# Kernel optimization log

Measured on AMD Instinct MI355X. Metric: run time of the kernel, lower is better.

## Reference

```python
import jax, jax.numpy as jnp
import numpy as np
import math

B, S, D, H, DFF = 4, 2048, 1024, 16, 4096
DK = D // H
EPS = 1e-5


def setup_inputs() -> dict:
    key = jax.random.key(0)
    ks = jax.random.split(key, 12)
    sc = 0.02
    inp = {
        "x": jax.random.normal(ks[0], (B, S, D), dtype=jnp.float32),
        "mask": jnp.ones((B, 1, 1, S), dtype=jnp.int32),
        "Wq": jax.random.normal(ks[1], (D, D), jnp.float32) * sc,
        "bq": jnp.zeros((D,), jnp.float32),
        "Wk": jax.random.normal(ks[2], (D, D), jnp.float32) * sc,
        "bk": jnp.zeros((D,), jnp.float32),
        "Wv": jax.random.normal(ks[3], (D, D), jnp.float32) * sc,
        "bv": jnp.zeros((D,), jnp.float32),
        "Wo": jax.random.normal(ks[4], (D, D), jnp.float32) * sc,
        "bo": jnp.zeros((D,), jnp.float32),
        "ln1_g": jnp.ones((D,), jnp.float32),
        "ln1_b": jnp.zeros((D,), jnp.float32),
        "W1": jax.random.normal(ks[5], (D, DFF), jnp.float32) * sc,
        "b1": jnp.zeros((DFF,), jnp.float32),
        "W2": jax.random.normal(ks[6], (DFF, D), jnp.float32) * sc,
        "b2": jnp.zeros((D,), jnp.float32),
        "ln2_g": jnp.ones((D,), jnp.float32),
        "ln2_b": jnp.zeros((D,), jnp.float32),
    }
    return inp


def _layer_norm(x, g, b):
    m = jnp.mean(x, axis=-1, keepdims=True)
    v = jnp.mean(jnp.square(x - m), axis=-1, keepdims=True)
    return (x - m) * jax.lax.rsqrt(v + EPS) * g + b


def reference(x, mask, Wq, bq, Wk, bk, Wv, bv, Wo, bo,
              ln1_g, ln1_b, W1, b1, W2, b2, ln2_g, ln2_b):
    b_, s_, d_ = x.shape
    h_, dk_ = H, DK
    # --- pre-LN attention sublayer ---
    hidden = _layer_norm(x, ln1_g, ln1_b)
    q = (hidden @ Wq + bq).reshape(b_, s_, h_, dk_).transpose(0, 2, 1, 3)  # [B,H,S,dk]
    k = (hidden @ Wk + bk).reshape(b_, s_, h_, dk_).transpose(0, 2, 1, 3)  # [B,H,S,dk]
    # NOTE: original code passes value=key (the value projection is dead code),
    # so K is used both as keys and as values. Reproduced faithfully.
    scores = jnp.einsum("bhqd,bhkd->bhqk", q, k) / math.sqrt(dk_)  # [B,H,S,S]
    scores = jnp.where(mask == 0, jnp.float32(-1e9), scores)
    p_attn = jax.nn.softmax(scores, axis=-1)
    attn_out = jnp.einsum("bhqk,bhkd->bhqd", p_attn, k)  # values == k
    attn_out = attn_out.transpose(0, 2, 1, 3).reshape(b_, s_, d_)
    attn_out = attn_out @ Wo + bo
    x = x + attn_out  # residual (dropout is identity in eval)
    # --- pre-LN FFN sublayer ---
    hidden2 = _layer_norm(x, ln2_g, ln2_b)
    ff = jax.nn.gelu(hidden2 @ W1 + b1, approximate=False) @ W2 + b2
    return x + ff
```

## Files before the change

kernel.cpp:

```cpp
#include <hip/hip_runtime.h>
#include <hip/hip_bf16.h>
#include <math.h>

#define B_   4
#define S_   2048
#define D_   1024
#define H_   16
#define DK_  64
#define DFF_ 4096
#define M_   (B_*S_)

typedef __bf16 bf16;
typedef bf16 bf16x8 __attribute__((ext_vector_type(8)));
typedef bf16 bf16x4 __attribute__((ext_vector_type(4)));
typedef float f32x4 __attribute__((ext_vector_type(4)));

__device__ __forceinline__ void g2lds16(const void* g, void* l) {
  __builtin_amdgcn_global_load_lds(
      (__attribute__((address_space(1))) void*)(void*)g,
      (__attribute__((address_space(3))) void*)l, 16, 0, 0);
}

__device__ __forceinline__ void* swzp(char* base, int row, int byteofs) {
  return base + row * 128 + (byteofs ^ ((row & 7) << 4));
}

__global__ void tcast_all(const float* __restrict__ Wq, const float* __restrict__ Wk,
                          const float* __restrict__ Wo, const float* __restrict__ W1,
                          const float* __restrict__ W2,
                          bf16* __restrict__ WqkT, bf16* __restrict__ WoT,
                          bf16* __restrict__ W1T, bf16* __restrict__ W2T) {
  __shared__ float t[32][33];
  int bid = blockIdx.x;
  const float* src; bf16* dst; int K, N, bx, by;
  if (bid < 1024)      { src = Wq; dst = WqkT;            K = 1024; N = 1024; bx = bid & 31;  by = bid >> 5; }
  else if (bid < 2048) { bid -= 1024; src = Wk; dst = WqkT + 1024 * 1024; K = 1024; N = 1024; bx = bid & 31;  by = bid >> 5; }
  else if (bid < 3072) { bid -= 2048; src = Wo; dst = WoT; K = 1024; N = 1024; bx = bid & 31;  by = bid >> 5; }
  else if (bid < 7168) { bid -= 3072; src = W1; dst = W1T; K = 1024; N = 4096; bx = bid & 127; by = bid >> 7; }
  else                 { bid -= 7168; src = W2; dst = W2T; K = 4096; N = 1024; bx = bid & 31;  by = bid >> 5; }
  int n0 = bx * 32, k0 = by * 32;
  int tx = threadIdx.x, ty = threadIdx.y;
#pragma unroll
  for (int i = 0; i < 4; ++i)
    t[ty + i*8][tx] = src[(size_t)(k0 + ty + i*8) * N + n0 + tx];
  __syncthreads();
#pragma unroll
  for (int i = 0; i < 4; ++i)
    dst[(size_t)(n0 + ty + i*8) * K + k0 + tx] = (bf16)t[tx][ty + i*8];
}

__global__ __launch_bounds__(256)
void ktrans(const bf16* __restrict__ Kt, bf16* __restrict__ KT) {
  __shared__ bf16 t[64][72];
  const int bh = blockIdx.y, s0 = blockIdx.x * 64, tid = threadIdx.x;
  const bf16* src = Kt + (size_t)bh * S_ * DK_;
  bf16* dst = KT + (size_t)bh * DK_ * S_;
#pragma unroll
  for (int i = 0; i < 2; ++i) {
    int c = tid * 2 + i;
    int r = c >> 3, col = (c & 7) * 8;
    *(bf16x8*)&t[r][col] = *(const bf16x8*)&src[(size_t)(s0 + r) * 64 + col];
  }
  __syncthreads();
  const int d = tid >> 2, sc = (tid & 3) * 16;
  bf16x8 v0, v1;
#pragma unroll
  for (int j = 0; j < 8; ++j) { v0[j] = t[sc + j][d]; v1[j] = t[sc + 8 + j][d]; }
  *(bf16x8*)&dst[(size_t)d * S_ + s0 + sc] = v0;
  *(bf16x8*)&dst[(size_t)d * S_ + s0 + sc + 8] = v1;
}

__global__ __launch_bounds__(256)
void ln_fwd(const float* __restrict__ x, const float* __restrict__ g,
            const float* __restrict__ be, bf16* __restrict__ out) {
  int row = blockIdx.x, tid = threadIdx.x;
  const float4 v = *(const float4*)&x[(size_t)row * D_ + tid * 4];
  float s = v.x + v.y + v.z + v.w;
  float q = v.x*v.x + v.y*v.y + v.z*v.z + v.w*v.w;
#pragma unroll
  for (int d = 32; d; d >>= 1) { s += __shfl_down(s, d); q += __shfl_down(q, d); }
  __shared__ float red[8];
  int wave = tid >> 6, lane = tid & 63;
  if (lane == 0) { red[wave*2] = s; red[wave*2+1] = q; }
  __syncthreads();
  float ts = red[0] + red[2] + red[4] + red[6];
  float tq = red[1] + red[3] + red[5] + red[7];
  float mean = ts * (1.0f / D_);
  float var  = tq * (1.0f / D_) - mean * mean;
  float rstd = rsqrtf(var + 1e-5f);
  const float4 gg = *(const float4*)&g[tid * 4];
  const float4 bb = *(const float4*)&be[tid * 4];
  bf16x4 ov;
  ov[0] = (bf16)((v.x - mean) * rstd * gg.x + bb.x);
  ov[1] = (bf16)((v.y - mean) * rstd * gg.y + bb.y);
  ov[2] = (bf16)((v.z - mean) * rstd * gg.z + bb.z);
  ov[3] = (bf16)((v.w - mean) * rstd * gg.w + bb.w);
  *(bf16x4*)&out[(size_t)row * D_ + tid * 4] = ov;
}

template <int EPI>
__global__ __launch_bounds__(256)
void gemm_bt(const bf16* __restrict__ A, const bf16* __restrict__ Bt,
             int M, int N, int K,
             const float* __restrict__ bias, const float* __restrict__ bias2,
             const float* __restrict__ resid, float scale,
             float* __restrict__ outf, bf16* __restrict__ outb,
             bf16* __restrict__ outb2) {
  __shared__ __align__(16) bf16 As[128 * 32];
  __shared__ __align__(16) bf16 Bs[128 * 32];
  const int tid = threadIdx.x;
  const int wave = tid >> 6, lane = tid & 63;
  const int wr = wave >> 1, wc = wave & 1;

  const int gx = gridDim.x, nwg = gx * gridDim.y;
  int wg = blockIdx.y * gx + blockIdx.x;
  wg = (wg & 7) * (nwg >> 3) + (wg >> 3);
  const long arow = (long)(wg / gx) * 128;
  const long bcol = (long)(wg % gx) * 128;

  f32x4 acc[4][4] = {};

  const int c0 = wave * 2, c1 = wave * 2 + 1;
  const int srow0 = c0 * 16 + (lane >> 2);
  const int srow1 = c1 * 16 + (lane >> 2);
  const int scol = (lane & 3) * 8;
  const int l15 = lane & 15, kof = (lane >> 4) * 8;

  for (int k0 = 0; k0 < K; k0 += 32) {
    g2lds16(A  + (arow + srow0) * (long)K + k0 + scol, &As[c0 * 512]);
    g2lds16(A  + (arow + srow1) * (long)K + k0 + scol, &As[c1 * 512]);
    g2lds16(Bt + (bcol + srow0) * (long)K + k0 + scol, &Bs[c0 * 512]);
    g2lds16(Bt + (bcol + srow1) * (long)K + k0 + scol, &Bs[c1 * 512]);
    __syncthreads();
    bf16x8 a[4], b[4];
#pragma unroll
    for (int i = 0; i < 4; ++i)
      a[i] = *(const bf16x8*)&As[(wr * 64 + i * 16 + l15) * 32 + kof];
#pragma unroll
    for (int i = 0; i < 4; ++i)
      b[i] = *(const bf16x8*)&Bs[(wc * 64 + i * 16 + l15) * 32 + kof];
#pragma unroll
    for (int mi = 0; mi < 4; ++mi)
#pragma unroll
      for (int ni = 0; ni < 4; ++ni)
        acc[mi][ni] = __builtin_amdgcn_mfma_f32_16x16x32_bf16(
            a[mi], b[ni], acc[mi][ni], 0, 0, 0);
    __syncthreads();
  }

#pragma unroll
  for (int mi = 0; mi < 4; ++mi) {
#pragma unroll
    for (int ni = 0; ni < 4; ++ni) {
#pragma unroll
      for (int j = 0; j < 4; ++j) {
        long row = arow + wr * 64 + mi * 16 + (lane >> 4) * 4 + j;
        long col = bcol + wc * 64 + ni * 16 + l15;
        float v = acc[mi][ni][j];
        if constexpr (EPI == 0) {
          int bb = (int)(row >> 11), ss = (int)(row & 2047);
          int hh = (int)(col >> 6) & 15, dd = (int)(col & 63);
          size_t idx = (((size_t)(bb * H_ + hh)) * S_ + ss) * DK_ + dd;
          if (col < 1024) outb[idx]  = (bf16)((v + bias[col]) * scale);
          else            outb2[idx] = (bf16)(v + bias2[col - 1024]);
        } else if constexpr (EPI == 1) {
          size_t idx = (size_t)row * N + col;
          outf[idx] = v + bias[col] + resid[idx];
        } else {
          size_t idx = (size_t)row * N + col;
          float t = v + bias[col];
          outb[idx] = (bf16)(0.5f * t * (1.0f + erff(t * 0.70710678118654752f)));
        }
      }
    }
  }
}

__global__ __launch_bounds__(256)
void attn_fwd(const bf16* __restrict__ Q, const bf16* __restrict__ Kk,
              const bf16* __restrict__ KT, const int* __restrict__ mask,
              bf16* __restrict__ O) {
  __shared__ __align__(16) char Kl[64 * 128];
  __shared__ __align__(16) char Vl[64 * 128];
  __shared__ __align__(16) char Pl[4][16 * 128];

  const int tid = threadIdx.x, wave = tid >> 6, lane = tid & 63;
  const int bh = blockIdx.y, b = bh >> 4, h = bh & 15;
  const int q0 = blockIdx.x * 64;
  const int l15 = lane & 15, q4 = lane >> 4;

  const bf16* Qp = Q  + (size_t)bh * S_ * DK_;
  const bf16* Kp = Kk + (size_t)bh * S_ * DK_;
  const bf16* Tp = KT + (size_t)bh * DK_ * S_;

  const int qrow = q0 + wave * 16 + l15;
  const bf16x8 qf0 = *(const bf16x8*)&Qp[(size_t)qrow * 64 + q4 * 8];
  const bf16x8 qf1 = *(const bf16x8*)&Qp[(size_t)qrow * 64 + 32 + q4 * 8];

  const int c0 = tid * 2, c1 = tid * 2 + 1;
  const int sr0 = c0 >> 3, sb0 = c0 & 7;
  const int sr1 = c1 >> 3, sb1 = c1 & 7;

  int poff[16];
#pragma unroll
  for (int nt = 0; nt < 4; ++nt)
#pragma unroll
    for (int j = 0; j < 4; ++j) {
      int r = q4 * 4 + j;
      poff[nt * 4 + j] = r * 128 + ((((nt * 16 + l15) * 2)) ^ ((r & 7) << 4));
    }

  bf16x8 onesv;
#pragma unroll
  for (int i = 0; i < 8; ++i) onesv[i] = (bf16)1.0f;

  f32x4 o[4] = {};
  f32x4 ol = {};
  float m_r[4];
#pragma unroll
  for (int j = 0; j < 4; ++j) m_r[j] = -__builtin_inff();

  bf16x8 a0 = *(const bf16x8*)&Kp[(size_t)sr0 * 64 + sb0 * 8];
  bf16x8 a1 = *(const bf16x8*)&Kp[(size_t)sr1 * 64 + sb1 * 8];
  bf16x8 t0 = *(const bf16x8*)&Tp[(size_t)sr0 * S_ + sb0 * 8];
  bf16x8 t1 = *(const bf16x8*)&Tp[(size_t)sr1 * S_ + sb1 * 8];

  for (int k0 = 0; k0 < S_; k0 += 64) {
    *(bf16x8*)swzp(Kl, sr0, sb0 * 16) = a0;
    *(bf16x8*)swzp(Kl, sr1, sb1 * 16) = a1;
    *(bf16x8*)swzp(Vl, sr0, sb0 * 16) = t0;
    *(bf16x8*)swzp(Vl, sr1, sb1 * 16) = t1;
    __syncthreads();

    const int nk = k0 + 64;
    if (nk < S_) {
      a0 = *(const bf16x8*)&Kp[(size_t)(nk + sr0) * 64 + sb0 * 8];
      a1 = *(const bf16x8*)&Kp[(size_t)(nk + sr1) * 64 + sb1 * 8];
      t0 = *(const bf16x8*)&Tp[(size_t)sr0 * S_ + nk + sb0 * 8];
      t1 = *(const bf16x8*)&Tp[(size_t)sr1 * S_ + nk + sb1 * 8];
    }

    const int mv = mask[b * S_ + k0 + lane];
    const bool anyz = __any(mv == 0);

    f32x4 s[4];
#pragma unroll
    for (int nt = 0; nt < 4; ++nt) {
      bf16x8 kf0 = *(const bf16x8*)swzp(Kl, nt * 16 + l15, q4 * 16);
      bf16x8 kf1 = *(const bf16x8*)swzp(Kl, nt * 16 + l15, 64 + q4 * 16);
      f32x4 z = {};
      z     = __builtin_amdgcn_mfma_f32_16x16x32_bf16(qf0, kf0, z, 0, 0, 0);
      s[nt] = __builtin_amdgcn_mfma_f32_16x16x32_bf16(qf1, kf1, z, 0, 0, 0);
    }
    if (anyz) {
#pragma unroll
      for (int nt = 0; nt < 4; ++nt) {
        int m2 = mask[b * S_ + k0 + nt * 16 + l15];
        if (m2 == 0) {
#pragma unroll
          for (int j = 0; j < 4; ++j) s[nt][j] = -1e9f;
        }
      }
    }

    float tm[4];
#pragma unroll
    for (int j = 0; j < 4; ++j)
      tm[j] = fmaxf(fmaxf(s[0][j], s[1][j]), fmaxf(s[2][j], s[3][j]));
#pragma unroll
    for (int d = 1; d < 16; d <<= 1)
#pragma unroll
      for (int j = 0; j < 4; ++j)
        tm[j] = fmaxf(tm[j], __shfl_xor(tm[j], d));

    bool ok = true;
#pragma unroll
    for (int j = 0; j < 4; ++j) ok = ok && (tm[j] <= m_r[j] + 8.0f);
    if (!__all(ok)) {
#pragma unroll
      for (int j = 0; j < 4; ++j) {
        float mn = fmaxf(m_r[j], tm[j]);
        float sf = __builtin_amdgcn_exp2f(m_r[j] - mn);
        m_r[j] = mn;
        ol[j] *= sf;
#pragma unroll
        for (int nf = 0; nf < 4; ++nf) o[nf][j] *= sf;
      }
    }

#pragma unroll
    for (int nt = 0; nt < 4; ++nt)
#pragma unroll
      for (int j = 0; j < 4; ++j)
        *(bf16*)(&Pl[wave][0] + poff[nt * 4 + j]) =
            (bf16)__builtin_amdgcn_exp2f(s[nt][j] - m_r[j]);

    const bf16x8 pf0 = *(const bf16x8*)swzp(Pl[wave], l15, q4 * 16);
    const bf16x8 pf1 = *(const bf16x8*)swzp(Pl[wave], l15, 64 + q4 * 16);

    ol = __builtin_amdgcn_mfma_f32_16x16x32_bf16(pf0, onesv, ol, 0, 0, 0);
    ol = __builtin_amdgcn_mfma_f32_16x16x32_bf16(pf1, onesv, ol, 0, 0, 0);

#pragma unroll
    for (int nf = 0; nf < 4; ++nf) {
      bf16x8 vf0 = *(const bf16x8*)swzp(Vl, nf * 16 + l15, q4 * 16);
      bf16x8 vf1 = *(const bf16x8*)swzp(Vl, nf * 16 + l15, 64 + q4 * 16);
      o[nf] = __builtin_amdgcn_mfma_f32_16x16x32_bf16(pf0, vf0, o[nf], 0, 0, 0);
      o[nf] = __builtin_amdgcn_mfma_f32_16x16x32_bf16(pf1, vf1, o[nf], 0, 0, 0);
    }
    __syncthreads();
  }

#pragma unroll
  for (int nf = 0; nf < 4; ++nf)
#pragma unroll
    for (int j = 0; j < 4; ++j) {
      int row = q0 + wave * 16 + q4 * 4 + j;
      int col = h * 64 + nf * 16 + l15;
      O[((size_t)b * S_ + row) * D_ + col] = (bf16)(o[nf][j] / ol[j]);
    }
}

extern "C" void kernel_launch(void* const* d_in, const int* in_sizes, int n_in,
                              void* d_out, int out_size, void* d_ws, size_t ws_size,
                              hipStream_t stream) {
  const float* x    = (const float*)d_in[0];
  const int*   mask = (const int*)d_in[1];
  const float* Wq   = (const float*)d_in[2];
  const float* bq   = (const float*)d_in[3];
  const float* Wk   = (const float*)d_in[4];
  const float* bk   = (const float*)d_in[5];
  const float* Wo   = (const float*)d_in[8];
  const float* bo   = (const float*)d_in[9];
  const float* ln1g = (const float*)d_in[10];
  const float* ln1b = (const float*)d_in[11];
  const float* W1   = (const float*)d_in[12];
  const float* b1   = (const float*)d_in[13];
  const float* W2   = (const float*)d_in[14];
  const float* b2   = (const float*)d_in[15];
  const float* ln2g = (const float*)d_in[16];
  const float* ln2b = (const float*)d_in[17];
  float* out = (float*)d_out;

  char* w = (char*)d_ws;
  auto alloc = [&](size_t bytes) {
    void* p = (void*)w;
    w += (bytes + 255) & ~(size_t)255;
    return p;
  };
  bf16* xln  = (bf16*)alloc((size_t)M_ * D_ * 2);
  bf16* WqkT = (bf16*)alloc((size_t)2 * D_ * D_ * 2);
  bf16* WoT  = (bf16*)alloc((size_t)D_ * D_ * 2);
  bf16* W1T  = (bf16*)alloc((size_t)D_ * DFF_ * 2);
  bf16* W2T  = (bf16*)alloc((size_t)D_ * DFF_ * 2);
  bf16* Qt   = (bf16*)alloc((size_t)M_ * D_ * 2);
  bf16* Kt   = (bf16*)alloc((size_t)M_ * D_ * 2);
  bf16* KTt  = (bf16*)alloc((size_t)M_ * D_ * 2);
  bf16* attn = (bf16*)alloc((size_t)M_ * D_ * 2);
  float* x2  = (float*)alloc((size_t)M_ * D_ * 4);
  bf16* h2   = (bf16*)alloc((size_t)M_ * D_ * 2);
  bf16* act  = (bf16*)alloc((size_t)M_ * DFF_ * 2);

  tcast_all<<<11264, dim3(32, 8), 0, stream>>>(Wq, Wk, Wo, W1, W2,
                                               WqkT, WoT, W1T, W2T);

  ln_fwd<<<M_, 256, 0, stream>>>(x, ln1g, ln1b, xln);

  gemm_bt<0><<<dim3(16, 64), 256, 0, stream>>>(
      xln, WqkT, M_, 2048, 1024, bq, bk, nullptr,
      0.125f * 1.4426950408889634f, nullptr, Qt, Kt);

  ktrans<<<dim3(S_ / 64, B_ * H_), 256, 0, stream>>>(Kt, KTt);

  attn_fwd<<<dim3(S_ / 64, B_ * H_), 256, 0, stream>>>(Qt, Kt, KTt, mask, attn);

  gemm_bt<1><<<dim3(8, 64), 256, 0, stream>>>(attn, WoT, M_, 1024, 1024,
                                              bo, nullptr, x, 1.0f,
                                              x2, nullptr, nullptr);

  ln_fwd<<<M_, 256, 0, stream>>>(x2, ln2g, ln2b, h2);

  gemm_bt<2><<<dim3(32, 64), 256, 0, stream>>>(h2, W1T, M_, 4096, 1024,
                                               b1, nullptr, nullptr, 1.0f,
                                               nullptr, act, nullptr);
  gemm_bt<1><<<dim3(8, 64), 256, 0, stream>>>(act, W2T, M_, 1024, 4096,
                                              b2, nullptr, x2, 1.0f,
                                              out, nullptr, nullptr);
}
```

Measured before the change: 661.5 us.

## Double-buffer LDS tiles in GEMM and attention, hoist mask check

The GEMM main loop now uses two LDS buffers for A and B. The next k-tile is issued with global_load_lds before the MFMAs on the current tile, so loads overlap compute with one barrier per iteration. Attention gets the same treatment for K/V: the prefetched registers are written into the alternate LDS buffer after the PV MFMAs, which removes the second barrier per iteration. Two smaller changes in attention: the mask-zero test is done once per block with __syncthreads_or instead of every tile, and the cross-lane row-max shuffle reduction only runs inside the rare rescale branch. The cost is double the LDS footprint, which may reduce occupancy.

Measured after the change: 597.7 us. -9.7%, faster.

```diff
diff --git a/kernel.cpp b/kernel.cpp
--- a/kernel.cpp
+++ b/kernel.cpp
@@ -106,8 +106,8 @@
              const float* __restrict__ resid, float scale,
              float* __restrict__ outf, bf16* __restrict__ outb,
              bf16* __restrict__ outb2) {
-  __shared__ __align__(16) bf16 As[128 * 32];
-  __shared__ __align__(16) bf16 Bs[128 * 32];
+  __shared__ __align__(16) bf16 As[2][128 * 32];
+  __shared__ __align__(16) bf16 Bs[2][128 * 32];
   const int tid = threadIdx.x;
   const int wave = tid >> 6, lane = tid & 63;
   const int wr = wave >> 1, wc = wave & 1;
@@ -126,19 +126,25 @@
   const int scol = (lane & 3) * 8;
   const int l15 = lane & 15, kof = (lane >> 4) * 8;
 
+  auto stage = [&](int buf, int k0) {
+    g2lds16(A  + (arow + srow0) * (long)K + k0 + scol, &As[buf][c0 * 512]);
+    g2lds16(A  + (arow + srow1) * (long)K + k0 + scol, &As[buf][c1 * 512]);
+    g2lds16(Bt + (bcol + srow0) * (long)K + k0 + scol, &Bs[buf][c0 * 512]);
+    g2lds16(Bt + (bcol + srow1) * (long)K + k0 + scol, &Bs[buf][c1 * 512]);
+  };
+
+  stage(0, 0);
+  __syncthreads();
+  int cur = 0;
   for (int k0 = 0; k0 < K; k0 += 32) {
-    g2lds16(A  + (arow + srow0) * (long)K + k0 + scol, &As[c0 * 512]);
-    g2lds16(A  + (arow + srow1) * (long)K + k0 + scol, &As[c1 * 512]);
-    g2lds16(Bt + (bcol + srow0) * (long)K + k0 + scol, &Bs[c0 * 512]);
-    g2lds16(Bt + (bcol + srow1) * (long)K + k0 + scol, &Bs[c1 * 512]);
-    __syncthreads();
+    if (k0 + 32 < K) stage(cur ^ 1, k0 + 32);
     bf16x8 a[4], b[4];
 #pragma unroll
     for (int i = 0; i < 4; ++i)
-      a[i] = *(const bf16x8*)&As[(wr * 64 + i * 16 + l15) * 32 + kof];
+      a[i] = *(const bf16x8*)&As[cur][(wr * 64 + i * 16 + l15) * 32 + kof];
 #pragma unroll
     for (int i = 0; i < 4; ++i)
-      b[i] = *(const bf16x8*)&Bs[(wc * 64 + i * 16 + l15) * 32 + kof];
+      b[i] = *(const bf16x8*)&Bs[cur][(wc * 64 + i * 16 + l15) * 32 + kof];
 #pragma unroll
     for (int mi = 0; mi < 4; ++mi)
 #pragma unroll
@@ -146,6 +152,7 @@
         acc[mi][ni] = __builtin_amdgcn_mfma_f32_16x16x32_bf16(
             a[mi], b[ni], acc[mi][ni], 0, 0, 0);
     __syncthreads();
+    cur ^= 1;
   }
 
 #pragma unroll
@@ -180,8 +187,8 @@
 void attn_fwd(const bf16* __restrict__ Q, const bf16* __restrict__ Kk,
               const bf16* __restrict__ KT, const int* __restrict__ mask,
               bf16* __restrict__ O) {
-  __shared__ __align__(16) char Kl[64 * 128];
-  __shared__ __align__(16) char Vl[64 * 128];
+  __shared__ __align__(16) char Kl[2][64 * 128];
+  __shared__ __align__(16) char Vl[2][64 * 128];
   __shared__ __align__(16) char Pl[4][16 * 128];
 
   const int tid = threadIdx.x, wave = tid >> 6, lane = tid & 63;
@@ -197,6 +204,10 @@
   const bf16x8 qf0 = *(const bf16x8*)&Qp[(size_t)qrow * 64 + q4 * 8];
   const bf16x8 qf1 = *(const bf16x8*)&Qp[(size_t)qrow * 64 + 32 + q4 * 8];
 
+  int lz = 0;
+  for (int i = tid; i < S_; i += 256) lz |= (mask[b * S_ + i] == 0);
+  const bool anyz = __syncthreads_or(lz) != 0;
+
   const int c0 = tid * 2, c1 = tid * 2 + 1;
   const int sr0 = c0 >> 3, sb0 = c0 & 7;
   const int sr1 = c1 >> 3, sb1 = c1 & 7;
@@ -224,12 +235,13 @@
   bf16x8 a1 = *(const bf16x8*)&Kp[(size_t)sr1 * 64 + sb1 * 8];
   bf16x8 t0 = *(const bf16x8*)&Tp[(size_t)sr0 * S_ + sb0 * 8];
   bf16x8 t1 = *(const bf16x8*)&Tp[(size_t)sr1 * S_ + sb1 * 8];
+  *(bf16x8*)swzp(Kl[0], sr0, sb0 * 16) = a0;
+  *(bf16x8*)swzp(Kl[0], sr1, sb1 * 16) = a1;
+  *(bf16x8*)swzp(Vl[0], sr0, sb0 * 16) = t0;
+  *(bf16x8*)swzp(Vl[0], sr1, sb1 * 16) = t1;
+  int cur = 0;
 
   for (int k0 = 0; k0 < S_; k0 += 64) {
-    *(bf16x8*)swzp(Kl, sr0, sb0 * 16) = a0;
-    *(bf16x8*)swzp(Kl, sr1, sb1 * 16) = a1;
-    *(bf16x8*)swzp(Vl, sr0, sb0 * 16) = t0;
-    *(bf16x8*)swzp(Vl, sr1, sb1 * 16) = t1;
     __syncthreads();
 
     const int nk = k0 + 64;
@@ -240,14 +252,11 @@
       t1 = *(const bf16x8*)&Tp[(size_t)sr1 * S_ + nk + sb1 * 8];
     }
 
-    const int mv = mask[b * S_ + k0 + lane];
-    const bool anyz = __any(mv == 0);
-
     f32x4 s[4];
 #pragma unroll
     for (int nt = 0; nt < 4; ++nt) {
-      bf16x8 kf0 = *(const bf16x8*)swzp(Kl, nt * 16 + l15, q4 * 16);
-      bf16x8 kf1 = *(const bf16x8*)swzp(Kl, nt * 16 + l15, 64 + q4 * 16);
+      bf16x8 kf0 = *(const bf16x8*)swzp(Kl[cur], nt * 16 + l15, q4 * 16);
+      bf16x8 kf1 = *(const bf16x8*)swzp(Kl[cur], nt * 16 + l15, 64 + q4 * 16);
       f32x4 z = {};
       z     = __builtin_amdgcn_mfma_f32_16x16x32_bf16(qf0, kf0, z, 0, 0, 0);
       s[nt] = __builtin_amdgcn_mfma_f32_16x16x32_bf16(qf1, kf1, z, 0, 0, 0);
@@ -267,16 +276,15 @@
 #pragma unroll
     for (int j = 0; j < 4; ++j)
       tm[j] = fmaxf(fmaxf(s[0][j], s[1][j]), fmaxf(s[2][j], s[3][j]));
-#pragma unroll
-    for (int d = 1; d < 16; d <<= 1)
-#pragma unroll
-      for (int j = 0; j < 4; ++j)
-        tm[j] = fmaxf(tm[j], __shfl_xor(tm[j], d));
-
     bool ok = true;
 #pragma unroll
     for (int j = 0; j < 4; ++j) ok = ok && (tm[j] <= m_r[j] + 8.0f);
     if (!__all(ok)) {
+#pragma unroll
+      for (int d = 1; d < 16; d <<= 1)
+#pragma unroll
+        for (int j = 0; j < 4; ++j)
+          tm[j] = fmaxf(tm[j], __shfl_xor(tm[j], d));
 #pragma unroll
       for (int j = 0; j < 4; ++j) {
         float mn = fmaxf(m_r[j], tm[j]);
@@ -303,12 +311,19 @@
 
 #pragma unroll
     for (int nf = 0; nf < 4; ++nf) {
-      bf16x8 vf0 = *(const bf16x8*)swzp(Vl, nf * 16 + l15, q4 * 16);
-      bf16x8 vf1 = *(const bf16x8*)swzp(Vl, nf * 16 + l15, 64 + q4 * 16);
+      bf16x8 vf0 = *(const bf16x8*)swzp(Vl[cur], nf * 16 + l15, q4 * 16);
+      bf16x8 vf1 = *(const bf16x8*)swzp(Vl[cur], nf * 16 + l15, 64 + q4 * 16);
       o[nf] = __builtin_amdgcn_mfma_f32_16x16x32_bf16(pf0, vf0, o[nf], 0, 0, 0);
       o[nf] = __builtin_amdgcn_mfma_f32_16x16x32_bf16(pf1, vf1, o[nf], 0, 0, 0);
     }
-    __syncthreads();
+
+    if (nk < S_) {
+      *(bf16x8*)swzp(Kl[cur ^ 1], sr0, sb0 * 16) = a0;
+      *(bf16x8*)swzp(Kl[cur ^ 1], sr1, sb1 * 16) = a1;
+      *(bf16x8*)swzp(Vl[cur ^ 1], sr0, sb0 * 16) = t0;
+      *(bf16x8*)swzp(Vl[cur ^ 1], sr1, sb1 * 16) = t1;
+    }
+    cur ^= 1;
   }
 
 #pragma unroll
```
